# Performance work log

Hardware: AMD Instinct MI355X
Metric: run time of the kernel (lower is better)

The kernel has to match this reference:

```python
import jax, jax.numpy as jnp
import numpy as np

B, K, V = 64, 8, 128000

def setup_inputs() -> dict:
    key = jax.random.key(0)
    ks = jax.random.split(key, 6)
    # probs are normalized distributions over the vocab, as produced by softmax upstream
    draft_probs = jax.nn.softmax(jax.random.normal(ks[0], (B, K, V), dtype=jnp.float32), axis=-1)
    oracle_probs = jax.nn.softmax(jax.random.normal(ks[1], (B, K + 1, V), dtype=jnp.float32), axis=-1)
    draft_tokens = jax.random.randint(ks[2], (B, K), 0, V, dtype=jnp.int32)
    oracle_tokens = jax.random.randint(ks[3], (B, K), 0, V, dtype=jnp.int32)
    uniforms = jax.random.uniform(ks[4], (B, K), dtype=jnp.float32)   # accept/reject draws (torch.rand per step)
    sample_u = jax.random.uniform(ks[5], (B,), dtype=jnp.float32)     # draw for residual/bonus sample
    return {
        'draft_tokens': draft_tokens,
        'draft_probs': draft_probs,
        'oracle_tokens': oracle_tokens,
        'oracle_probs': oracle_probs,
        'uniforms': uniforms,
        'sample_u': sample_u,
        'num_draft_tokens': K,
    }

def reference(draft_tokens, draft_probs, oracle_tokens, oracle_probs, uniforms, sample_u, num_draft_tokens):
    # Parallel-prefix formulation of the sequential accept/reject loop.
    Kd = num_draft_tokens
    bidx = jnp.arange(draft_probs.shape[0])
    # p_draft[i] = draft_probs[i, draft_token_i], p_oracle[i] = oracle_probs[i, draft_token_i]
    p_d = jnp.take_along_axis(draft_probs, draft_tokens[..., None], axis=-1)[..., 0]          # [B,K]
    p_o = jnp.take_along_axis(oracle_probs[:, :Kd], draft_tokens[..., None], axis=-1)[..., 0]  # [B,K]
    accept_prob = jnp.minimum(1.0, p_o / p_d)                                                  # [B,K]
    accept = uniforms < accept_prob                                                            # [B,K]
    # number of accepted tokens = length of leading run of accepts (loop breaks at first reject)
    prefix = jnp.cumprod(accept.astype(jnp.int32), axis=1)
    num_accepted = prefix.sum(axis=1)                                                          # [B]
    all_accepted = num_accepted == Kd
    # residual distribution at the first rejected position r (clipped when all accepted)
    r = jnp.minimum(num_accepted, Kd - 1)
    o_r = oracle_probs[bidx, r]                                                                # [B,V]
    d_r = draft_probs[bidx, r]                                                                 # [B,V]
    residual = jnp.maximum(o_r - d_r, 0.0)
    residual = residual / residual.sum(axis=-1, keepdims=True)
    bonus_dist = oracle_probs[:, Kd]                                                           # [B,V]
    final_dist = jnp.where(all_accepted[:, None], bonus_dist, residual)
    # inverse-CDF sample of the replacement/bonus token
    cdf = jnp.cumsum(final_dist, axis=-1)
    new_token = jnp.minimum(jnp.sum(cdf < sample_u[:, None], axis=-1), final_dist.shape[-1] - 1).astype(jnp.int32)
    # pack accepted prefix + sampled token, pad with -1 to fixed length K+1
    pos = jnp.arange(Kd + 1)[None, :]
    draft_pad = jnp.pad(draft_tokens, ((0, 0), (0, 1)))
    tokens = jnp.where(pos < num_accepted[:, None], draft_pad,
                       jnp.where(pos == num_accepted[:, None], new_token[:, None], -1)).astype(jnp.int32)
    return tokens, num_accepted
```

## Files before the change

kernel.cpp:

```cpp
#include <hip/hip_runtime.h>

#define B 64
#define K 8
#define V 128000
#define CH 4096
#define NCH 32

__global__ __launch_bounds__(64) void k1_accept(
    const int*   __restrict__ draft_tokens,
    const float* __restrict__ draft_probs,
    const float* __restrict__ oracle_probs,
    const float* __restrict__ uniforms,
    int* __restrict__ meta,
    int* __restrict__ out_na)
{
  int b = threadIdx.x;
  if (b >= B) return;
  int na = 0;
  for (int k = 0; k < K; ++k) {
    int t   = draft_tokens[b * K + k];
    float pd = draft_probs [((size_t)(b * K       + k)) * V + t];
    float po = oracle_probs[((size_t)(b * (K + 1) + k)) * V + t];
    float ap = fminf(1.0f, po / pd);
    if (uniforms[b * K + k] < ap) na++; else break;
  }
  meta[b]   = na;
  out_na[b] = na;
}

__global__ __launch_bounds__(256) void k2_sums(
    const float* __restrict__ draft_probs,
    const float* __restrict__ oracle_probs,
    const int*   __restrict__ meta,
    float* __restrict__ chunkSums)
{
  const int b = blockIdx.x >> 5;
  const int c = blockIdx.x & 31;
  const int na  = meta[b];
  const bool acc = (na == K);
  const int row = acc ? K : na;
  const float* orow = oracle_probs + ((size_t)(b * (K + 1) + row)) * V;
  const float* drow = draft_probs  + ((size_t)(b * K       + row)) * V;

  const int base = c * CH;
  float s = 0.f;
#pragma unroll
  for (int it = 0; it < 4; ++it) {
    int idx = base + it * 1024 + (int)threadIdx.x * 4;
    if (idx < V) {
      float4 o = *(const float4*)(orow + idx);
      if (acc) {
        s += (o.x + o.y) + (o.z + o.w);
      } else {
        float4 d = *(const float4*)(drow + idx);
        s += fmaxf(o.x - d.x, 0.f) + fmaxf(o.y - d.y, 0.f)
           + fmaxf(o.z - d.z, 0.f) + fmaxf(o.w - d.w, 0.f);
      }
    }
  }
  for (int off = 32; off > 0; off >>= 1) s += __shfl_down(s, off);
  __shared__ float wsum[4];
  int lane = threadIdx.x & 63, w = threadIdx.x >> 6;
  if (lane == 0) wsum[w] = s;
  __syncthreads();
  if (threadIdx.x == 0)
    chunkSums[b * NCH + c] = (wsum[0] + wsum[1]) + (wsum[2] + wsum[3]);
}

__global__ __launch_bounds__(256) void k3_sample(
    const int*   __restrict__ draft_tokens,
    const float* __restrict__ draft_probs,
    const float* __restrict__ oracle_probs,
    const float* __restrict__ sample_u,
    const int*   __restrict__ meta,
    const float* __restrict__ chunkSums,
    int* __restrict__ out_tokens)
{
  const int b    = blockIdx.x;
  const int tid  = threadIdx.x;
  const int lane = tid & 63, w = tid >> 6;

  const int na   = meta[b];
  const bool acc = (na == K);
  const int row  = acc ? K : na;
  const float* orow = oracle_probs + ((size_t)(b * (K + 1) + row)) * V;
  const float* drow = draft_probs  + ((size_t)(b * K       + row)) * V;

  __shared__ float sT, sBase;
  __shared__ int   sC, sIdx;
  __shared__ float sWS[4];

  if (w == 0) {
    float v = (lane < NCH) ? chunkSums[b * NCH + lane] : 0.f;
    float incl = v;
    for (int off = 1; off < NCH; off <<= 1) {
      float n = __shfl_up(incl, off);
      if (lane >= off) incl += n;
    }
    float S = __shfl(incl, NCH - 1);
    float T = acc ? sample_u[b] : sample_u[b] * S;
    unsigned long long m = __ballot(lane < NCH && incl >= T);
    if (lane == 0) {
      sT = T;
      if (m == 0ULL) { sC = -1; sIdx = V - 1; sBase = 0.f; }
    }
    if (m != 0ULL) {
      int cstar = __ffsll((long long)m) - 1;
      if (lane == cstar) {
        sC = cstar;
        sBase = incl - v;
        int fb = cstar * CH + CH - 1;
        sIdx = fb < V ? fb : V - 1;
      }
    }
  }
  __syncthreads();

  const int cstar = sC;
  int new_token;
  if (cstar >= 0) {
    const float T = sT;
    const int base = cstar * CH;
    const int estart = base + tid * 16;
    float vals[16];
    float s = 0.f;
#pragma unroll
    for (int j4 = 0; j4 < 4; ++j4) {
      int idx = estart + j4 * 4;
      float4 o = make_float4(0.f, 0.f, 0.f, 0.f);
      float4 d = make_float4(0.f, 0.f, 0.f, 0.f);
      if (idx < V) {
        o = *(const float4*)(orow + idx);
        if (!acc) d = *(const float4*)(drow + idx);
      }
      float v0 = acc ? o.x : fmaxf(o.x - d.x, 0.f);
      float v1 = acc ? o.y : fmaxf(o.y - d.y, 0.f);
      float v2 = acc ? o.z : fmaxf(o.z - d.z, 0.f);
      float v3 = acc ? o.w : fmaxf(o.w - d.w, 0.f);
      vals[j4 * 4 + 0] = v0; vals[j4 * 4 + 1] = v1;
      vals[j4 * 4 + 2] = v2; vals[j4 * 4 + 3] = v3;
      s += (v0 + v1) + (v2 + v3);
    }
    float incl = s;
    for (int off = 1; off < 64; off <<= 1) {
      float n = __shfl_up(incl, off);
      if (lane >= off) incl += n;
    }
    if (lane == 63) sWS[w] = incl;
    __syncthreads();
    float woff = 0.f;
    for (int i = 0; i < w; ++i) woff += sWS[i];
    float run = sBase + woff + (incl - s);
    int found = -1;
#pragma unroll
    for (int j = 0; j < 16; ++j) {
      run += vals[j];
      if (found < 0 && run >= T) found = estart + j;
    }
    if (found >= 0 && found < V) atomicMin(&sIdx, found);
    __syncthreads();
    new_token = sIdx;
  } else {
    new_token = V - 1;
  }

  if (tid < K + 1) {
    int pos = tid, val;
    if (pos < na)       val = draft_tokens[b * K + pos];
    else if (pos == na) val = new_token;
    else                val = -1;
    out_tokens[b * (K + 1) + pos] = val;
  }
}

extern "C" void kernel_launch(void* const* d_in, const int* in_sizes, int n_in,
                              void* d_out, int out_size, void* d_ws, size_t ws_size,
                              hipStream_t stream) {
  const int*   draft_tokens = (const int*)  d_in[0];
  const float* draft_probs  = (const float*)d_in[1];
  const float* oracle_probs = (const float*)d_in[3];
  const float* uniforms     = (const float*)d_in[4];
  const float* sample_u     = (const float*)d_in[5];

  int* out_tokens = (int*)d_out;
  int* out_na     = out_tokens + B * (K + 1);

  float* chunkSums = (float*)d_ws;
  int*   meta      = (int*)d_ws + B * NCH;

  k1_accept<<<1, 64, 0, stream>>>(draft_tokens, draft_probs, oracle_probs,
                                  uniforms, meta, out_na);
  k2_sums<<<B * NCH, 256, 0, stream>>>(draft_probs, oracle_probs, meta, chunkSums);
  k3_sample<<<B, 256, 0, stream>>>(draft_tokens, draft_probs, oracle_probs,
                                   sample_u, meta, chunkSums, out_tokens);
}
```

Before: 457.0 us.

## Fuse chunk-sum and sampling kernels via last-block atomic counter; parallelize accept

Merges the chunk-sum and sampling kernels into one launch. Each block atomically increments a per-batch counter after writing its chunk sum, and the last block for that batch does the prefix scan and the inverse-CDF search. The accept kernel now handles all 512 (b,k) pairs in parallel, using a ballot to find the first reject and zeroing the counters. This removes one kernel launch and the serial per-row gather chain, at the cost of threadfence and atomic overhead and a serialized tail block per batch.

```diff
diff --git a/kernel.cpp b/kernel.cpp
--- a/kernel.cpp
+++ b/kernel.cpp
@@ -6,39 +6,52 @@
 #define CH 4096
 #define NCH 32
 
-__global__ __launch_bounds__(64) void k1_accept(
+
+__global__ __launch_bounds__(512) void k_init(
     const int*   __restrict__ draft_tokens,
     const float* __restrict__ draft_probs,
     const float* __restrict__ oracle_probs,
     const float* __restrict__ uniforms,
     int* __restrict__ meta,
+    int* __restrict__ counters,
     int* __restrict__ out_na)
 {
-  int b = threadIdx.x;
-  if (b >= B) return;
-  int na = 0;
-  for (int k = 0; k < K; ++k) {
-    int t   = draft_tokens[b * K + k];
-    float pd = draft_probs [((size_t)(b * K       + k)) * V + t];
-    float po = oracle_probs[((size_t)(b * (K + 1) + k)) * V + t];
-    float ap = fminf(1.0f, po / pd);
-    if (uniforms[b * K + k] < ap) na++; else break;
-  }
-  meta[b]   = na;
-  out_na[b] = na;
+  const int tid = threadIdx.x;
+  if (tid < B) counters[tid] = 0;
+
+  const int b = tid >> 3;
+  const int k = tid & 7;
+  int   t  = draft_tokens[b * K + k];
+  float pd = draft_probs [((size_t)(b * K       + k)) * V + t];
+  float po = oracle_probs[((size_t)(b * (K + 1) + k)) * V + t];
+  bool accept = uniforms[b * K + k] < fminf(1.0f, po / pd);
+
+  unsigned long long mask = __ballot(accept);
+  const int g = (tid >> 3) & 7;
+  unsigned m8 = (unsigned)((mask >> (g * 8)) & 0xFFull);
+  int na = __ffs((~m8) & 0x1FF) - 1;
+
+  if (k == 0) { meta[b] = na; out_na[b] = na; }
 }
 
-__global__ __launch_bounds__(256) void k2_sums(
+__global__ __launch_bounds__(256) void k_fused(
+    const int*   __restrict__ draft_tokens,
     const float* __restrict__ draft_probs,
     const float* __restrict__ oracle_probs,
+    const float* __restrict__ sample_u,
     const int*   __restrict__ meta,
-    float* __restrict__ chunkSums)
+    float* __restrict__ chunkSums,
+    int*   __restrict__ counters,
+    int*   __restrict__ out_tokens)
 {
-  const int b = blockIdx.x >> 5;
-  const int c = blockIdx.x & 31;
-  const int na  = meta[b];
+  const int b    = blockIdx.x >> 5;
+  const int c    = blockIdx.x & 31;
+  const int tid  = threadIdx.x;
+  const int lane = tid & 63, w = tid >> 6;
+
+  const int na   = meta[b];
   const bool acc = (na == K);
-  const int row = acc ? K : na;
+  const int row  = acc ? K : na;
   const float* orow = oracle_probs + ((size_t)(b * (K + 1) + row)) * V;
   const float* drow = draft_probs  + ((size_t)(b * K       + row)) * V;
 
@@ -46,7 +59,7 @@
   float s = 0.f;
 #pragma unroll
   for (int it = 0; it < 4; ++it) {
-    int idx = base + it * 1024 + (int)threadIdx.x * 4;
+    int idx = base + it * 1024 + tid * 4;
     if (idx < V) {
       float4 o = *(const float4*)(orow + idx);
       if (acc) {
@@ -60,31 +73,19 @@
   }
   for (int off = 32; off > 0; off >>= 1) s += __shfl_down(s, off);
   __shared__ float wsum[4];
-  int lane = threadIdx.x & 63, w = threadIdx.x >> 6;
   if (lane == 0) wsum[w] = s;
   __syncthreads();
-  if (threadIdx.x == 0)
+
+  __shared__ int sLastFlag;
+  if (tid == 0) {
     chunkSums[b * NCH + c] = (wsum[0] + wsum[1]) + (wsum[2] + wsum[3]);
-}
-
-__global__ __launch_bounds__(256) void k3_sample(
-    const int*   __restrict__ draft_tokens,
-    const float* __restrict__ draft_probs,
-    const float* __restrict__ oracle_probs,
-    const float* __restrict__ sample_u,
-    const int*   __restrict__ meta,
-    const float* __restrict__ chunkSums,
-    int* __restrict__ out_tokens)
-{
-  const int b    = blockIdx.x;
-  const int tid  = threadIdx.x;
-  const int lane = tid & 63, w = tid >> 6;
-
-  const int na   = meta[b];
-  const bool acc = (na == K);
-  const int row  = acc ? K : na;
-  const float* orow = oracle_probs + ((size_t)(b * (K + 1) + row)) * V;
-  const float* drow = draft_probs  + ((size_t)(b * K       + row)) * V;
+    __threadfence();
+    int old = atomicAdd(&counters[b], 1);
+    sLastFlag = (old == NCH - 1) ? 1 : 0;
+  }
+  __syncthreads();
+  if (sLastFlag == 0) return;
+  __threadfence();
 
   __shared__ float sT, sBase;
   __shared__ int   sC, sIdx;
@@ -120,10 +121,10 @@
   int new_token;
   if (cstar >= 0) {
     const float T = sT;
-    const int base = cstar * CH;
-    const int estart = base + tid * 16;
+    const int cbase = cstar * CH;
+    const int estart = cbase + tid * 16;
     float vals[16];
-    float s = 0.f;
+    float s2 = 0.f;
 #pragma unroll
     for (int j4 = 0; j4 < 4; ++j4) {
       int idx = estart + j4 * 4;
@@ -139,9 +140,9 @@
       float v3 = acc ? o.w : fmaxf(o.w - d.w, 0.f);
       vals[j4 * 4 + 0] = v0; vals[j4 * 4 + 1] = v1;
       vals[j4 * 4 + 2] = v2; vals[j4 * 4 + 3] = v3;
-      s += (v0 + v1) + (v2 + v3);
+      s2 += (v0 + v1) + (v2 + v3);
     }
-    float incl = s;
+    float incl = s2;
     for (int off = 1; off < 64; off <<= 1) {
       float n = __shfl_up(incl, off);
       if (lane >= off) incl += n;
@@ -150,7 +151,7 @@
     __syncthreads();
     float woff = 0.f;
     for (int i = 0; i < w; ++i) woff += sWS[i];
-    float run = sBase + woff + (incl - s);
+    float run = sBase + woff + (incl - s2);
     int found = -1;
 #pragma unroll
     for (int j = 0; j < 16; ++j) {
@@ -187,10 +188,11 @@
 
   float* chunkSums = (float*)d_ws;
   int*   meta      = (int*)d_ws + B * NCH;
+  int*   counters  = meta + B;
 
-  k1_accept<<<1, 64, 0, stream>>>(draft_tokens, draft_probs, oracle_probs,
-                                  uniforms, meta, out_na);
-  k2_sums<<<B * NCH, 256, 0, stream>>>(draft_probs, oracle_probs, meta, chunkSums);
-  k3_sample<<<B, 256, 0, stream>>>(draft_tokens, draft_probs, oracle_probs,
-                                   sample_u, meta, chunkSums, out_tokens);
+  k_init <<<1, 512, 0, stream>>>(draft_tokens, draft_probs, oracle_probs,
+                                 uniforms, meta, counters, out_na);
+  k_fused<<<B * NCH, 256, 0, stream>>>(draft_tokens, draft_probs, oracle_probs,
+                                       sample_u, meta, chunkSums, counters,
+                                       out_tokens);
 }
```

Result: slower. 563.5 us (+23.3%).
